# Kernel optimization log

Measured on AMD Instinct MI355X. Metric: run time of the kernel, lower is better.

Reference implementation:

```python
import jax, jax.numpy as jnp
import numpy as np

N_NODES = 100000
N_EDGES = 1600000
DIMS = [64, 64, 64, 32]  # [n_feat] + hid


def setup_inputs() -> dict:
    key = jax.random.key(0)
    ks = jax.random.split(key, 2 + 2 * (len(DIMS) - 1))
    x = jax.random.normal(ks[0], (N_NODES, DIMS[0]), dtype=jnp.float32)
    edge_index = jax.random.randint(ks[1], (2, N_EDGES), 0, N_NODES, dtype=jnp.int64)
    inp = {"x": x, "edge_index": edge_index}
    for i in range(len(DIMS) - 1):
        fan_in, fan_out = DIMS[i], DIMS[i + 1]
        scale = 1.0 / np.sqrt(fan_in)
        inp[f"W{i+1}"] = jax.random.normal(ks[2 + 2 * i], (fan_in, fan_out), dtype=jnp.float32) * scale
        inp[f"b{i+1}"] = jax.random.normal(ks[3 + 2 * i], (fan_out,), dtype=jnp.float32) * scale
    return inp


def _gcn_conv(x, W, b, src, dst, dis):
    # h = X W ; out[i] = sum_{j->i} norm_ij * h[j] + dis[i]^2 * h[i] + b
    h = x @ W
    norm = dis[src] * dis[dst]                      # [E]
    agg = jax.ops.segment_sum(h[src] * norm[:, None], dst, num_segments=x.shape[0])
    agg = agg + h * (dis * dis)[:, None]            # self-loop contribution
    return agg + b


def reference(x, edge_index, W1, b1, W2, b2, W3, b3):
    src, dst = edge_index[0], edge_index[1]
    n = x.shape[0]
    # degree with self-loops (edge weight 1), symmetric normalization
    deg = jax.ops.segment_sum(jnp.ones(src.shape[0], x.dtype), dst, num_segments=n) + 1.0
    dis = jax.lax.rsqrt(deg)
    h = jax.nn.relu(_gcn_conv(x, W1, b1, src, dst, dis))   # dropout is identity in eval
    h = jax.nn.relu(_gcn_conv(h, W2, b2, src, dst, dis))
    return _gcn_conv(h, W3, b3, src, dst, dis)
```

## Files before the change

### kernel.cpp

```cpp
#include <hip/hip_runtime.h>


typedef __attribute__((ext_vector_type(8))) _Float16 half8;
typedef __attribute__((ext_vector_type(4))) _Float16 half4;

static inline int cdiv(int a, int b) { return (a + b - 1) / b; }

#define ACHUNK 8192
#define MAXNBK 512

__global__ void k_bucket_hist(const int* __restrict__ dst, int* __restrict__ counts_t,
                              int NBK, int NBA, int E) {
    __shared__ int cnt[MAXNBK];
    int t = threadIdx.x, b = blockIdx.x;
    for (int i = t; i < NBK; i += 256) cnt[i] = 0;
    __syncthreads();
    int e0 = b * ACHUNK;
#pragma unroll 8
    for (int j = 0; j < ACHUNK / 256; ++j) {
        int e = e0 + j * 256 + t;
        if (e < E) atomicAdd(&cnt[dst[e] >> 8], 1);
    }
    __syncthreads();
    for (int i = t; i < NBK; i += 256) counts_t[i * NBA + b] = cnt[i];
}

#define SCAN_T 256
#define SCAN_V 4
#define SCAN_CHUNK 1024

__global__ void k_scan_partial(const int* __restrict__ a, int* __restrict__ bsum, int n) {
    __shared__ int red[SCAN_T];
    int t = threadIdx.x, b = blockIdx.x;
    int base = b * SCAN_CHUNK + t * SCAN_V;
    int s = 0;
#pragma unroll
    for (int j = 0; j < SCAN_V; ++j) { int i = base + j; if (i < n) s += a[i]; }
    red[t] = s;
    __syncthreads();
    for (int off = SCAN_T / 2; off > 0; off >>= 1) {
        if (t < off) red[t] += red[t + off];
        __syncthreads();
    }
    if (t == 0) bsum[b] = red[0];
}

__global__ void k_scan_final(const int* __restrict__ a, const int* __restrict__ bsum,
                             int* __restrict__ out, int nb, int n) {
    __shared__ int sb[256];
    __shared__ int sh[SCAN_T];
    int t = threadIdx.x, bk = blockIdx.x;
    sb[t] = (t < nb) ? bsum[t] : 0;
    __syncthreads();
    for (int off = 1; off < 256; off <<= 1) {
        int u = (t >= off) ? sb[t - off] : 0;
        __syncthreads();
        sb[t] += u;
        __syncthreads();
    }
    int bbase = (bk == 0) ? 0 : sb[bk - 1];
    int base = bk * SCAN_CHUNK + t * SCAN_V;
    int v[SCAN_V];
    int s = 0;
#pragma unroll
    for (int j = 0; j < SCAN_V; ++j) {
        int i = base + j;
        v[j] = (i < n) ? a[i] : 0;
        s += v[j];
    }
    sh[t] = s;
    __syncthreads();
    for (int off = 1; off < SCAN_T; off <<= 1) {
        int u = (t >= off) ? sh[t - off] : 0;
        __syncthreads();
        sh[t] += u;
        __syncthreads();
    }
    int run = sh[t] - s + bbase;
#pragma unroll
    for (int j = 0; j < SCAN_V; ++j) {
        int i = base + j;
        if (i < n) { out[i] = run; run += v[j]; }
    }
}

__global__ void k_bucket_scatter(const int* __restrict__ src, const int* __restrict__ dst,
                                 const int* __restrict__ offsets, unsigned* __restrict__ bucketed,
                                 int NBK, int NBA, int E) {
    __shared__ int curs[MAXNBK];
    int t = threadIdx.x, b = blockIdx.x;
    for (int i = t; i < NBK; i += 256) curs[i] = offsets[i * NBA + b];
    __syncthreads();
    int e0 = b * ACHUNK;
#pragma unroll 8
    for (int j = 0; j < ACHUNK / 256; ++j) {
        int e = e0 + j * 256 + t;
        if (e < E) {
            int d = dst[e];
            int pos = atomicAdd(&curs[d >> 8], 1);
            bucketed[pos] = (unsigned)src[e] | ((unsigned)(d & 255) << 24);
        }
    }
}

__global__ void k_bucket_build(const unsigned* __restrict__ bucketed,
                               const int* __restrict__ offsets,
                               int* __restrict__ csr_src, int* __restrict__ row_start,
                               float* __restrict__ dis, int NBK, int NBA, int N, int E) {
    __shared__ int cnt[256];
    __shared__ int sc[256];
    int t = threadIdx.x, k = blockIdx.x;
    int base = offsets[k * NBA];
    int end = (k + 1 < NBK) ? offsets[(k + 1) * NBA] : E;
    cnt[t] = 0;
    __syncthreads();
    for (int i = base + t; i < end; i += 256)
        atomicAdd(&cnt[bucketed[i] >> 24], 1);
    __syncthreads();
    int c = cnt[t];
    sc[t] = c;
    __syncthreads();
    for (int off = 1; off < 256; off <<= 1) {
        int u = (t >= off) ? sc[t - off] : 0;
        __syncthreads();
        sc[t] += u;
        __syncthreads();
    }
    int excl = sc[t] - c;
    int node = k * 256 + t;
    if (node < N) {
        row_start[node] = base + excl;
        dis[node] = rsqrtf(1.0f + (float)c);
    }
    if (k == 0 && t == 0) row_start[N] = E;
    cnt[t] = base + excl;
    __syncthreads();
    for (int i = base + t; i < end; i += 256) {
        unsigned w = bucketed[i];
        int pos = atomicAdd(&cnt[w >> 24], 1);
        csr_src[pos] = (int)(w & 0xFFFFFFu);
    }
}

template <int K, int M>
__global__ void k_gemm_f(const float* __restrict__ X, const float* __restrict__ W,
                         const float* __restrict__ dis, _Float16* __restrict__ H, int n) {
    constexpr int TPR = M / 8;
    constexpr int ROWS = 256 / TPR;
    constexpr int KP = K + 1;
    __shared__ float Ws[K * M];
    __shared__ float Xs[ROWS * KP];
    int tid = threadIdx.x;
    for (int idx = tid; idx < K * M / 4; idx += 256)
        ((float4*)Ws)[idx] = ((const float4*)W)[idx];
    int row0 = blockIdx.x * ROWS;
    for (int idx = tid; idx < ROWS * (K / 4); idx += 256) {
        int r = idx / (K / 4), kq = idx % (K / 4);
        int row = row0 + r;
        float4 vv = (row < n) ? ((const float4*)X)[(size_t)row * (K / 4) + kq]
                              : make_float4(0.f, 0.f, 0.f, 0.f);
        Xs[r * KP + kq * 4 + 0] = vv.x;
        Xs[r * KP + kq * 4 + 1] = vv.y;
        Xs[r * KP + kq * 4 + 2] = vv.z;
        Xs[r * KP + kq * 4 + 3] = vv.w;
    }
    __syncthreads();
    int r = tid / TPR, c0 = (tid % TPR) * 8;
    int row = row0 + r;
    if (row >= n) return;
    float4 a0 = make_float4(0.f, 0.f, 0.f, 0.f);
    float4 a1 = make_float4(0.f, 0.f, 0.f, 0.f);
#pragma unroll
    for (int k = 0; k < K; ++k) {
        float xv = Xs[r * KP + k];
        float4 w0 = ((const float4*)Ws)[(k * M + c0) / 4];
        float4 w1 = ((const float4*)Ws)[(k * M + c0) / 4 + 1];
        a0.x = fmaf(xv, w0.x, a0.x);
        a0.y = fmaf(xv, w0.y, a0.y);
        a0.z = fmaf(xv, w0.z, a0.z);
        a0.w = fmaf(xv, w0.w, a0.w);
        a1.x = fmaf(xv, w1.x, a1.x);
        a1.y = fmaf(xv, w1.y, a1.y);
        a1.z = fmaf(xv, w1.z, a1.z);
        a1.w = fmaf(xv, w1.w, a1.w);
    }
    float dn = dis[row];
    half8 hv;
    hv[0] = (_Float16)(a0.x * dn);
    hv[1] = (_Float16)(a0.y * dn);
    hv[2] = (_Float16)(a0.z * dn);
    hv[3] = (_Float16)(a0.w * dn);
    hv[4] = (_Float16)(a1.x * dn);
    hv[5] = (_Float16)(a1.y * dn);
    hv[6] = (_Float16)(a1.z * dn);
    hv[7] = (_Float16)(a1.w * dn);
    ((half8*)H)[(size_t)row * (M / 8) + c0 / 8] = hv;
}

template <int MOUT>
__global__ __launch_bounds__(256, 8)
void k_fused_agg_gemm(const _Float16* __restrict__ h, const float* __restrict__ dis,
                      const int* __restrict__ row_start, const int* __restrict__ csr_src,
                      const float* __restrict__ bagg, const float* __restrict__ W,
                      _Float16* __restrict__ H, int n) {
    constexpr int K = 64, KP = K + 1;
    __shared__ __align__(16) _Float16 Ws[K * MOUT];
    __shared__ float Xs[32 * KP];
    int tid = threadIdx.x;
    for (int idx = tid; idx < K * MOUT / 4; idx += 256) {
        float4 wv = ((const float4*)W)[idx];
        half4 h4;
        h4[0] = (_Float16)wv.x;
        h4[1] = (_Float16)wv.y;
        h4[2] = (_Float16)wv.z;
        h4[3] = (_Float16)wv.w;
        ((half4*)Ws)[idx] = h4;
    }

    int wave = tid >> 6, lane = tid & 63;
    int sub = lane >> 3, fl = lane & 7;
    int node0 = blockIdx.x * 32;
    int node = node0 + wave * 8 + sub;
    if (node < n) {
        const half8* h8 = (const half8*)h;
        float acc[8];
#pragma unroll
        for (int j = 0; j < 8; ++j) acc[j] = 0.f;
        int e = row_start[node], e1 = row_start[node + 1];
        for (; e + 7 < e1; e += 8) {
            int s0 = csr_src[e], s1 = csr_src[e + 1];
            int s2 = csr_src[e + 2], s3 = csr_src[e + 3];
// ... 16 lines not shown
            int s0 = csr_src[e], s1 = csr_src[e + 1];
            int s2 = csr_src[e + 2], s3 = csr_src[e + 3];
            half8 v0 = h8[(size_t)s0 * 8 + fl];
            half8 v1 = h8[(size_t)s1 * 8 + fl];
            half8 v2 = h8[(size_t)s2 * 8 + fl];
            half8 v3 = h8[(size_t)s3 * 8 + fl];
#pragma unroll
            for (int j = 0; j < 8; ++j)
                acc[j] += ((float)v0[j] + (float)v1[j]) + ((float)v2[j] + (float)v3[j]);
        }
        for (; e < e1; ++e) {
            int s0 = csr_src[e];
            half8 v0 = h8[(size_t)s0 * 8 + fl];
#pragma unroll
            for (int j = 0; j < 8; ++j) acc[j] += (float)v0[j];
        }
        float dn = dis[node];
        half8 hv = h8[(size_t)node * 8 + fl];
        float4 b0 = ((const float4*)bagg)[fl * 2];
        float4 b1 = ((const float4*)bagg)[fl * 2 + 1];
        int rrow = wave * 8 + sub;
        float* xp = &Xs[rrow * KP + fl * 8];
        xp[0] = fmaxf((acc[0] + (float)hv[0]) * dn + b0.x, 0.f);
        xp[1] = fmaxf((acc[1] + (float)hv[1]) * dn + b0.y, 0.f);
        xp[2] = fmaxf((acc[2] + (float)hv[2]) * dn + b0.z, 0.f);
        xp[3] = fmaxf((acc[3] + (float)hv[3]) * dn + b0.w, 0.f);
        xp[4] = fmaxf((acc[4] + (float)hv[4]) * dn + b1.x, 0.f);
        xp[5] = fmaxf((acc[5] + (float)hv[5]) * dn + b1.y, 0.f);
        xp[6] = fmaxf((acc[6] + (float)hv[6]) * dn + b1.z, 0.f);
        xp[7] = fmaxf((acc[7] + (float)hv[7]) * dn + b1.w, 0.f);
    }
    __syncthreads();

    constexpr int TPR = MOUT / 8;
    int r = tid / TPR, c0 = (tid % TPR) * 8;
    int row = node0 + r;
    if (r >= 32 || row >= n) return;
    float4 a0 = make_float4(0.f, 0.f, 0.f, 0.f);
    float4 a1 = make_float4(0.f, 0.f, 0.f, 0.f);
#pragma unroll
    for (int k = 0; k < K; ++k) {
        float xv = Xs[r * KP + k];
        half8 w = ((const half8*)Ws)[(k * MOUT + c0) / 8];
        a0.x = fmaf(xv, (float)w[0], a0.x);
        a0.y = fmaf(xv, (float)w[1], a0.y);
        a0.z = fmaf(xv, (float)w[2], a0.z);
        a0.w = fmaf(xv, (float)w[3], a0.w);
        a1.x = fmaf(xv, (float)w[4], a1.x);
        a1.y = fmaf(xv, (float)w[5], a1.y);
        a1.z = fmaf(xv, (float)w[6], a1.z);
        a1.w = fmaf(xv, (float)w[7], a1.w);
    }
    float dn = dis[row];
    half8 hv;
    hv[0] = (_Float16)(a0.x * dn);
    hv[1] = (_Float16)(a0.y * dn);
    hv[2] = (_Float16)(a0.z * dn);
    hv[3] = (_Float16)(a0.w * dn);
    hv[4] = (_Float16)(a1.x * dn);
    hv[5] = (_Float16)(a1.y * dn);
    hv[6] = (_Float16)(a1.z * dn);
    hv[7] = (_Float16)(a1.w * dn);
    ((half8*)H)[(size_t)row * (MOUT / 8) + c0 / 8] = hv;
}

__global__ __launch_bounds__(256, 8)
void k_aggregate32(const _Float16* __restrict__ h, const float* __restrict__ dis,
                   const int* __restrict__ row_start, const int* __restrict__ csr_src,
                   const float* __restrict__ b, float* __restrict__ out, int n) {
    constexpr int LPN = 4, NPW = 16;
    int gtid = blockIdx.x * blockDim.x + threadIdx.x;
    int wave = gtid >> 6;
    int lane = threadIdx.x & 63;
    int sub = lane / LPN, fl = lane % LPN;
    int node = wave * NPW + sub;
    if (node >= n) return;
    const half8* h8 = (const half8*)h;
    float acc[8];
#pragma unroll
    for (int j = 0; j < 8; ++j) acc[j] = 0.f;
    int e = row_start[node], e1 = row_start[node + 1];
    for (; e + 7 < e1; e += 8) {
        int s0 = csr_src[e], s1 = csr_src[e + 1];
        int s2 = csr_src[e + 2], s3 = csr_src[e + 3];
        int s4 = csr_src[e + 4], s5 = csr_src[e + 5];
        int s6 = csr_src[e + 6], s7 = csr_src[e + 7];
        half8 v0 = h8[(size_t)s0 * LPN + fl];
        half8 v1 = h8[(size_t)s1 * LPN + fl];
        half8 v2 = h8[(size_t)s2 * LPN + fl];
        half8 v3 = h8[(size_t)s3 * LPN + fl];
        half8 v4 = h8[(size_t)s4 * LPN + fl];
        half8 v5 = h8[(size_t)s5 * LPN + fl];
        half8 v6 = h8[(size_t)s6 * LPN + fl];
        half8 v7 = h8[(size_t)s7 * LPN + fl];
#pragma unroll
        for (int j = 0; j < 8; ++j)
// ... 20 lines not shown
    float dn = dis[node];
    half8 hv = h8[(size_t)node * LPN + fl];
    float4 b0 = ((const float4*)b)[fl * 2];
    float4 b1 = ((const float4*)b)[fl * 2 + 1];
    float4* op = (float4*)(out + ((size_t)node * LPN + fl) * 8);
    op[0] = make_float4((acc[0] + (float)hv[0]) * dn + b0.x,
                        (acc[1] + (float)hv[1]) * dn + b0.y,
                        (acc[2] + (float)hv[2]) * dn + b0.z,
                        (acc[3] + (float)hv[3]) * dn + b0.w);
    op[1] = make_float4((acc[4] + (float)hv[4]) * dn + b1.x,
                        (acc[5] + (float)hv[5]) * dn + b1.y,
                        (acc[6] + (float)hv[6]) * dn + b1.z,
                        (acc[7] + (float)hv[7]) * dn + b1.w);
}

extern "C" void kernel_launch(void* const* d_in, const int* in_sizes, int n_in,
                              void* d_out, int out_size, void* d_ws, size_t ws_size,
                              hipStream_t stream) {
    const float* x   = (const float*)d_in[0];
    const int*   ei  = (const int*)d_in[1];
    const float* W1  = (const float*)d_in[2];
    const float* b1  = (const float*)d_in[3];
    const float* W2  = (const float*)d_in[4];
    const float* b2  = (const float*)d_in[5];
    const float* W3  = (const float*)d_in[6];
    const float* b3  = (const float*)d_in[7];
    float* out = (float*)d_out;

    const int N = in_sizes[0] / 64;
    const int E = in_sizes[1] / 2;
    const int* src = ei;
    const int* dst = ei + E;

    const int NBK = cdiv(N, 256);
    const int NBA = cdiv(E, ACHUNK);
    const int nmat = NBK * NBA;

    const size_t Np = (size_t)((N + 63) / 64) * 64;
    char* p = (char*)d_ws;
    int*      counts_t = (int*)p;      p += (size_t)nmat * sizeof(int);
    int*      offsets  = (int*)p;      p += (size_t)nmat * sizeof(int);
    int*      bsum     = (int*)p;      p += 1024 * sizeof(int);
    int*      row_start= (int*)p;      p += (Np + 64) * sizeof(int);
    float*    dis      = (float*)p;    p += Np * sizeof(float);
    unsigned* bucketed = (unsigned*)p; p += (size_t)E * sizeof(unsigned);
    int*      csr_src  = (int*)p;      p += (size_t)E * sizeof(int);
    _Float16* bufA     = (_Float16*)p; p += Np * 64 * sizeof(_Float16);
    _Float16* bufB     = (_Float16*)p; p += Np * 64 * sizeof(_Float16);
    (void)ws_size;

    const int B = 256;
    const int nb = cdiv(nmat, SCAN_CHUNK);

    k_bucket_hist<<<NBA, B, 0, stream>>>(dst, counts_t, NBK, NBA, E);
    k_scan_partial<<<nb, B, 0, stream>>>(counts_t, bsum, nmat);
    k_scan_final<<<nb, B, 0, stream>>>(counts_t, bsum, offsets, nb, nmat);
    k_bucket_scatter<<<NBA, B, 0, stream>>>(src, dst, offsets, bucketed, NBK, NBA, E);
    k_bucket_build<<<NBK, B, 0, stream>>>(bucketed, offsets, csr_src, row_start, dis,
                                          NBK, NBA, N, E);

    k_gemm_f<64, 64><<<cdiv(N, 32), B, 0, stream>>>(x, W1, dis, bufA, N);
    k_fused_agg_gemm<64><<<cdiv(N, 32), B, 0, stream>>>(
        bufA, dis, row_start, csr_src, b1, W2, bufB, N);
    k_fused_agg_gemm<32><<<cdiv(N, 32), B, 0, stream>>>(
        bufB, dis, row_start, csr_src, b2, W3, bufA, N);
    k_aggregate32<<<cdiv(cdiv(N, 16) * 64, B), B, 0, stream>>>(
        bufA, dis, row_start, csr_src, b3, out, N);
}
```

Measured before the change: 302.2 us.

## Fuse CSR construction and first GEMM into one cooperative persistent kernel

Replaces the six separate kernels (histogram, two scan passes, bucket scatter, bucket build, first-layer GEMM) with one cooperative kernel that uses grid.sync between phases, aiming to cut launch and inter-kernel drain overhead. The bucket build now sorts each bucket in shared memory and writes csr_src coalesced, falling back to direct scatter for buckets too large to fit. The 32-output fused agg-gemm now uses all 256 threads with 4 columns each instead of leaving half the threads idle. Risks: the persistent grid may reduce parallelism in some phases, and each grid-wide barrier has its own cost.

```diff
diff --git a/kernel.cpp b/kernel.cpp
--- a/kernel.cpp
+++ b/kernel.cpp
@@ -1,5 +1,8 @@
 #include <hip/hip_runtime.h>
-
+#include <hip/hip_cooperative_groups.h>
+
+
+namespace cg = cooperative_groups;
 
 typedef __attribute__((ext_vector_type(8))) _Float16 half8;
 typedef __attribute__((ext_vector_type(4))) _Float16 half4;
@@ -8,6 +11,229 @@
 
 #define ACHUNK 8192
 #define MAXNBK 512
+#define SCAN_CHUNK 1024
+#define BCAP 6144
+#define SMEM_BYTES 26624
+
+__global__ __launch_bounds__(256)
+void k_csr_gemm(const int* __restrict__ src, const int* __restrict__ dst,
+                int* __restrict__ counts_t, int* __restrict__ offsets,
+                int* __restrict__ bsum, unsigned* __restrict__ bucketed,
+                int* __restrict__ csr_src, int* __restrict__ row_start,
+                float* __restrict__ dis, const float* __restrict__ X,
+                const float* __restrict__ W1, _Float16* __restrict__ H,
+                int NBK, int NBA, int nmat, int nb, int N, int E) {
+    cg::grid_group grid = cg::this_grid();
+    __shared__ __align__(16) char smem[SMEM_BYTES];
+    const int t = threadIdx.x;
+    const int nbl = gridDim.x;
+
+    {
+        int* cnt = (int*)smem;
+        for (int c = blockIdx.x; c < NBA; c += nbl) {
+            for (int i = t; i < NBK; i += 256) cnt[i] = 0;
+            __syncthreads();
+            int e0 = c * ACHUNK;
+#pragma unroll 8
+            for (int j = 0; j < ACHUNK / 256; ++j) {
+                int e = e0 + j * 256 + t;
+                if (e < E) atomicAdd(&cnt[dst[e] >> 8], 1);
+            }
+            __syncthreads();
+            for (int i = t; i < NBK; i += 256) counts_t[i * NBA + c] = cnt[i];
+            __syncthreads();
+        }
+    }
+    grid.sync();
+
+    {
+        int* red = (int*)smem;
+        for (int b = blockIdx.x; b < nb; b += nbl) {
+            int base = b * SCAN_CHUNK + t * 4;
+            int s = 0;
+#pragma unroll
+            for (int j = 0; j < 4; ++j) { int i = base + j; if (i < nmat) s += counts_t[i]; }
+            red[t] = s;
+            __syncthreads();
+            for (int off = 128; off > 0; off >>= 1) {
+                if (t < off) red[t] += red[t + off];
+                __syncthreads();
+            }
+            if (t == 0) bsum[b] = red[0];
+            __syncthreads();
+        }
+    }
+    grid.sync();
+
+    {
+        int* sb = (int*)smem;
+        int* sh = sb + 256;
+        for (int bk = blockIdx.x; bk < nb; bk += nbl) {
+            sb[t] = (t < nb) ? bsum[t] : 0;
+            __syncthreads();
+            for (int off = 1; off < 256; off <<= 1) {
+                int u = (t >= off) ? sb[t - off] : 0;
+                __syncthreads();
+                sb[t] += u;
+                __syncthreads();
+            }
+            int bbase = (bk == 0) ? 0 : sb[bk - 1];
+            int base = bk * SCAN_CHUNK + t * 4;
+            int v[4];
+            int s = 0;
+#pragma unroll
+            for (int j = 0; j < 4; ++j) {
+                int i = base + j;
+                v[j] = (i < nmat) ? counts_t[i] : 0;
+                s += v[j];
+            }
+            sh[t] = s;
+            __syncthreads();
+            for (int off = 1; off < 256; off <<= 1) {
+                int u = (t >= off) ? sh[t - off] : 0;
+                __syncthreads();
+                sh[t] += u;
+                __syncthreads();
+            }
+            int run = sh[t] - s + bbase;
+#pragma unroll
+            for (int j = 0; j < 4; ++j) {
+                int i = base + j;
+                if (i < nmat) { offsets[i] = run; run += v[j]; }
+            }
+            __syncthreads();
+        }
+    }
+    grid.sync();
+
+    {
+        int* curs = (int*)smem;
+        for (int c = blockIdx.x; c < NBA; c += nbl) {
+            for (int i = t; i < NBK; i += 256) curs[i] = offsets[i * NBA + c];
+            __syncthreads();
+            int e0 = c * ACHUNK;
+#pragma unroll 8
+            for (int j = 0; j < ACHUNK / 256; ++j) {
+                int e = e0 + j * 256 + t;
+                if (e < E) {
+                    int d = dst[e];
+                    int pos = atomicAdd(&curs[d >> 8], 1);
+                    bucketed[pos] = (unsigned)src[e] | ((unsigned)(d & 255) << 24);
+                }
+            }
+            __syncthreads();
+        }
+    }
+    grid.sync();
+
+    {
+        int* cnt = (int*)smem;
+        int* sc  = cnt + 256;
+        int* srt = sc + 256;
+        for (int k = blockIdx.x; k < NBK; k += nbl) {
+            int base = offsets[k * NBA];
+            int end = (k + 1 < NBK) ? offsets[(k + 1) * NBA] : E;
+            cnt[t] = 0;
+            __syncthreads();
+            for (int i = base + t; i < end; i += 256)
+                atomicAdd(&cnt[bucketed[i] >> 24], 1);
+            __syncthreads();
+            int c = cnt[t];
+            sc[t] = c;
+            __syncthreads();
+            for (int off = 1; off < 256; off <<= 1) {
+                int u = (t >= off) ? sc[t - off] : 0;
+                __syncthreads();
+                sc[t] += u;
+                __syncthreads();
+            }
+            int excl = sc[t] - c;
+            int node = k * 256 + t;
+            if (node < N) {
+                row_start[node] = base + excl;
+                dis[node] = rsqrtf(1.0f + (float)c);
+            }
+            if (k == 0 && t == 0) row_start[N] = E;
+            cnt[t] = excl;
+            __syncthreads();
+            int m = end - base;
+            if (m <= BCAP) {
+                for (int i = base + t; i < end; i += 256) {
+                    unsigned w = bucketed[i];
+                    int r = atomicAdd(&cnt[w >> 24], 1);
+                    srt[r] = (int)(w & 0xFFFFFFu);
+                }
+                __syncthreads();
+                for (int idx = t; idx < m; idx += 256)
+                    csr_src[base + idx] = srt[idx];
+            } else {
+                for (int i = base + t; i < end; i += 256) {
+                    unsigned w = bucketed[i];
+                    int pos = base + atomicAdd(&cnt[w >> 24], 1);
+                    csr_src[pos] = (int)(w & 0xFFFFFFu);
+                }
+            }
+            __syncthreads();
+        }
+    }
+    grid.sync();
+
+    {
+        float* Ws = (float*)smem;
+        float* Xs = Ws + 64 * 64;
+        constexpr int K = 64, KP = 65;
+        for (int idx = t; idx < K * 64 / 4; idx += 256)
+            ((float4*)Ws)[idx] = ((const float4*)W1)[idx];
+        int ntile = (N + 31) / 32;
+        int r = t / 8, c0 = (t % 8) * 8;
+        for (int tile = blockIdx.x; tile < ntile; tile += nbl) {
+            int row0 = tile * 32;
+            for (int idx = t; idx < 32 * (K / 4); idx += 256) {
+                int rr = idx / (K / 4), kq = idx % (K / 4);
+                int row = row0 + rr;
+                float4 vv = (row < N) ? ((const float4*)X)[(size_t)row * (K / 4) + kq]
+                                      : make_float4(0.f, 0.f, 0.f, 0.f);
+                Xs[rr * KP + kq * 4 + 0] = vv.x;
+                Xs[rr * KP + kq * 4 + 1] = vv.y;
+                Xs[rr * KP + kq * 4 + 2] = vv.z;
+                Xs[rr * KP + kq * 4 + 3] = vv.w;
+            }
+            __syncthreads();
+            int row = row0 + r;
+            if (row < N) {
+                float4 a0 = make_float4(0.f, 0.f, 0.f, 0.f);
+                float4 a1 = make_float4(0.f, 0.f, 0.f, 0.f);
+#pragma unroll
+                for (int k = 0; k < K; ++k) {
+                    float xv = Xs[r * KP + k];
+                    float4 w0 = ((const float4*)Ws)[(k * 64 + c0) / 4];
+                    float4 w1 = ((const float4*)Ws)[(k * 64 + c0) / 4 + 1];
+                    a0.x = fmaf(xv, w0.x, a0.x);
+                    a0.y = fmaf(xv, w0.y, a0.y);
+                    a0.z = fmaf(xv, w0.z, a0.z);
+                    a0.w = fmaf(xv, w0.w, a0.w);
+                    a1.x = fmaf(xv, w1.x, a1.x);
+                    a1.y = fmaf(xv, w1.y, a1.y);
+                    a1.z = fmaf(xv, w1.z, a1.z);
+                    a1.w = fmaf(xv, w1.w, a1.w);
+                }
+                float dn = dis[row];
+                half8 hv;
+                hv[0] = (_Float16)(a0.x * dn);
+                hv[1] = (_Float16)(a0.y * dn);
+                hv[2] = (_Float16)(a0.z * dn);
+                hv[3] = (_Float16)(a0.w * dn);
+                hv[4] = (_Float16)(a1.x * dn);
+                hv[5] = (_Float16)(a1.y * dn);
+                hv[6] = (_Float16)(a1.z * dn);
+                hv[7] = (_Float16)(a1.w * dn);
+                ((half8*)H)[(size_t)row * 8 + c0 / 8] = hv;
+            }
+            __syncthreads();
+        }
+    }
+}
+
 
 __global__ void k_bucket_hist(const int* __restrict__ dst, int* __restrict__ counts_t,
                               int NBK, int NBA, int E) {
@@ -25,20 +251,16 @@
     for (int i = t; i < NBK; i += 256) counts_t[i * NBA + b] = cnt[i];
 }
 
-#define SCAN_T 256
-#define SCAN_V 4
-#define SCAN_CHUNK 1024
-
 __global__ void k_scan_partial(const int* __restrict__ a, int* __restrict__ bsum, int n) {
-    __shared__ int red[SCAN_T];
+    __shared__ int red[256];
     int t = threadIdx.x, b = blockIdx.x;
-    int base = b * SCAN_CHUNK + t * SCAN_V;
+    int base = b * SCAN_CHUNK + t * 4;
     int s = 0;
 #pragma unroll
-    for (int j = 0; j < SCAN_V; ++j) { int i = base + j; if (i < n) s += a[i]; }
+    for (int j = 0; j < 4; ++j) { int i = base + j; if (i < n) s += a[i]; }
     red[t] = s;
     __syncthreads();
-    for (int off = SCAN_T / 2; off > 0; off >>= 1) {
+    for (int off = 128; off > 0; off >>= 1) {
         if (t < off) red[t] += red[t + off];
         __syncthreads();
     }
@@ -48,7 +270,7 @@
 __global__ void k_scan_final(const int* __restrict__ a, const int* __restrict__ bsum,
                              int* __restrict__ out, int nb, int n) {
     __shared__ int sb[256];
-    __shared__ int sh[SCAN_T];
+    __shared__ int sh[256];
     int t = threadIdx.x, bk = blockIdx.x;
     sb[t] = (t < nb) ? bsum[t] : 0;
     __syncthreads();
@@ -59,18 +281,18 @@
         __syncthreads();
     }
     int bbase = (bk == 0) ? 0 : sb[bk - 1];
-    int base = bk * SCAN_CHUNK + t * SCAN_V;
-    int v[SCAN_V];
+    int base = bk * SCAN_CHUNK + t * 4;
+    int v[4];
     int s = 0;
 #pragma unroll
-    for (int j = 0; j < SCAN_V; ++j) {
+    for (int j = 0; j < 4; ++j) {
         int i = base + j;
         v[j] = (i < n) ? a[i] : 0;
         s += v[j];
     }
     sh[t] = s;
     __syncthreads();
-    for (int off = 1; off < SCAN_T; off <<= 1) {
+    for (int off = 1; off < 256; off <<= 1) {
         int u = (t >= off) ? sh[t - off] : 0;
         __syncthreads();
         sh[t] += u;
@@ -78,7 +300,7 @@
     }
     int run = sh[t] - s + bbase;
 #pragma unroll
-    for (int j = 0; j < SCAN_V; ++j) {
+    for (int j = 0; j < 4; ++j) {
         int i = base + j;
         if (i < n) { out[i] = run; run += v[j]; }
     }
@@ -109,6 +331,7 @@
                                float* __restrict__ dis, int NBK, int NBA, int N, int E) {
     __shared__ int cnt[256];
     __shared__ int sc[256];
+    __shared__ int srt[BCAP];
     int t = threadIdx.x, k = blockIdx.x;
     int base = offsets[k * NBA];
     int end = (k + 1 < NBK) ? offsets[(k + 1) * NBA] : E;
@@ -133,12 +356,24 @@
         dis[node] = rsqrtf(1.0f + (float)c);
     }
     if (k == 0 && t == 0) row_start[N] = E;
-    cnt[t] = base + excl;
-    __syncthreads();
-    for (int i = base + t; i < end; i += 256) {
-        unsigned w = bucketed[i];
-        int pos = atomicAdd(&cnt[w >> 24], 1);
-        csr_src[pos] = (int)(w & 0xFFFFFFu);
+    cnt[t] = excl;
+    __syncthreads();
+    int m = end - base;
+    if (m <= BCAP) {
+        for (int i = base + t; i < end; i += 256) {
+            unsigned w = bucketed[i];
+            int r = atomicAdd(&cnt[w >> 24], 1);
+            srt[r] = (int)(w & 0xFFFFFFu);
+        }
+        __syncthreads();
+        for (int idx = t; idx < m; idx += 256)
+            csr_src[base + idx] = srt[idx];
+    } else {
+        for (int i = base + t; i < end; i += 256) {
+            unsigned w = bucketed[i];
+            int pos = base + atomicAdd(&cnt[w >> 24], 1);
+            csr_src[pos] = (int)(w & 0xFFFFFFu);
+        }
     }
 }
 
@@ -197,6 +432,7 @@
     ((half8*)H)[(size_t)row * (M / 8) + c0 / 8] = hv;
 }
 
+
 template <int MOUT>
 __global__ __launch_bounds__(256, 8)
 void k_fused_agg_gemm(const _Float16* __restrict__ h, const float* __restrict__ dis,
@@ -279,36 +515,54 @@
     }
     __syncthreads();
 
-    constexpr int TPR = MOUT / 8;
-    int r = tid / TPR, c0 = (tid % TPR) * 8;
+    constexpr int TPR = 8;
+    constexpr int CPT = MOUT / TPR;
+    int r = tid / TPR, c0 = (tid % TPR) * CPT;
     int row = node0 + r;
-    if (r >= 32 || row >= n) return;
+    if (row >= n) return;
     float4 a0 = make_float4(0.f, 0.f, 0.f, 0.f);
     float4 a1 = make_float4(0.f, 0.f, 0.f, 0.f);
 #pragma unroll
     for (int k = 0; k < K; ++k) {
         float xv = Xs[r * KP + k];
-        half8 w = ((const half8*)Ws)[(k * MOUT + c0) / 8];
-        a0.x = fmaf(xv, (float)w[0], a0.x);
-        a0.y = fmaf(xv, (float)w[1], a0.y);
-        a0.z = fmaf(xv, (float)w[2], a0.z);
-        a0.w = fmaf(xv, (float)w[3], a0.w);
-        a1.x = fmaf(xv, (float)w[4], a1.x);
-        a1.y = fmaf(xv, (float)w[5], a1.y);
-        a1.z = fmaf(xv, (float)w[6], a1.z);
-        a1.w = fmaf(xv, (float)w[7], a1.w);
+        if constexpr (CPT == 8) {
+            half8 w = ((const half8*)Ws)[(k * MOUT + c0) / 8];
+            a0.x = fmaf(xv, (float)w[0], a0.x);
+            a0.y = fmaf(xv, (float)w[1], a0.y);
+            a0.z = fmaf(xv, (float)w[2], a0.z);
+            a0.w = fmaf(xv, (float)w[3], a0.w);
+            a1.x = fmaf(xv, (float)w[4], a1.x);
+            a1.y = fmaf(xv, (float)w[5], a1.y);
+            a1.z = fmaf(xv, (float)w[6], a1.z);
+            a1.w = fmaf(xv, (float)w[7], a1.w);
+        } else {
+            half4 w = ((const half4*)Ws)[(k * MOUT + c0) / 4];
+            a0.x = fmaf(xv, (float)w[0], a0.x);
+            a0.y = fmaf(xv, (float)w[1], a0.y);
+            a0.z = fmaf(xv, (float)w[2], a0.z);
+            a0.w = fmaf(xv, (float)w[3], a0.w);
+        }
     }
     float dn = dis[row];
-    half8 hv;
-    hv[0] = (_Float16)(a0.x * dn);
-    hv[1] = (_Float16)(a0.y * dn);
-    hv[2] = (_Float16)(a0.z * dn);
-    hv[3] = (_Float16)(a0.w * dn);
-    hv[4] = (_Float16)(a1.x * dn);
-    hv[5] = (_Float16)(a1.y * dn);
-    hv[6] = (_Float16)(a1.z * dn);
-    hv[7] = (_Float16)(a1.w * dn);
-    ((half8*)H)[(size_t)row * (MOUT / 8) + c0 / 8] = hv;
+    if constexpr (CPT == 8) {
+        half8 hv;
+        hv[0] = (_Float16)(a0.x * dn);
+        hv[1] = (_Float16)(a0.y * dn);
+        hv[2] = (_Float16)(a0.z * dn);
+        hv[3] = (_Float16)(a0.w * dn);
+        hv[4] = (_Float16)(a1.x * dn);
+        hv[5] = (_Float16)(a1.y * dn);
+        hv[6] = (_Float16)(a1.z * dn);
+        hv[7] = (_Float16)(a1.w * dn);
+        ((half8*)H)[(size_t)row * (MOUT / 8) + c0 / 8] = hv;
+    } else {
+        half4 hv;
+        hv[0] = (_Float16)(a0.x * dn);
+        hv[1] = (_Float16)(a0.y * dn);
+        hv[2] = (_Float16)(a0.z * dn);
+        hv[3] = (_Float16)(a0.w * dn);
+        ((half4*)H)[(size_t)row * (MOUT / 4) + c0 / 4] = hv;
+    }
 }
 
 __global__ __launch_bounds__(256, 8)
@@ -398,6 +652,7 @@
     const int NBK = cdiv(N, 256);
     const int NBA = cdiv(E, ACHUNK);
     const int nmat = NBK * NBA;
+    const int nb = cdiv(nmat, SCAN_CHUNK);
 
     const size_t Np = (size_t)((N + 63) / 64) * 64;
     char* p = (char*)d_ws;
@@ -413,16 +668,50 @@
     (void)ws_size;
 
     const int B = 256;
-    const int nb = cdiv(nmat, SCAN_CHUNK);
-
-    k_bucket_hist<<<NBA, B, 0, stream>>>(dst, counts_t, NBK, NBA, E);
-    k_scan_partial<<<nb, B, 0, stream>>>(counts_t, bsum, nmat);
-    k_scan_final<<<nb, B, 0, stream>>>(counts_t, bsum, offsets, nb, nmat);
-    k_bucket_scatter<<<NBA, B, 0, stream>>>(src, dst, offsets, bucketed, NBK, NBA, E);
-    k_bucket_build<<<NBK, B, 0, stream>>>(bucketed, offsets, csr_src, row_start, dis,
-                                          NBK, NBA, N, E);
-
-    k_gemm_f<64, 64><<<cdiv(N, 32), B, 0, stream>>>(x, W1, dis, bufA, N);
+
+    static int coop_grid = -1;
+    if (coop_grid < 0) {
+        int dev = 0;
+        (void)hipGetDevice(&dev);
+        int ncu = 0;
+        (void)hipDeviceGetAttribute(&ncu, hipDeviceAttributeMultiprocessorCount, dev);
+        int maxb = 0;
+        (void)hipOccupancyMaxActiveBlocksPerMultiprocessor(
+            &maxb, (const void*)k_csr_gemm, B, 0);
+        long g = (long)maxb * (long)ncu;
+        if (g > 1024) g = 1024;
+        coop_grid = (int)g;
+    }
+
+    if (coop_grid >= 64) {
+        const int* src_a = src;
+        const int* dst_a = dst;
+        int* counts_a = counts_t;
+        int* offsets_a = offsets;
+        int* bsum_a = bsum;
+        unsigned* bucketed_a = bucketed;
+        int* csr_a = csr_src;
+        int* rs_a = row_start;
+        float* dis_a = dis;
+        const float* x_a = x;
+        const float* w1_a = W1;
+        _Float16* h_a = bufA;
+        int nbk_a = NBK, nba_a = NBA, nmat_a = nmat, nb_a = nb, n_a = N, e_a = E;
+        void* args[] = {&src_a, &dst_a, &counts_a, &offsets_a, &bsum_a,
+                        &bucketed_a, &csr_a, &rs_a, &dis_a, &x_a, &w1_a, &h_a,
+                        &nbk_a, &nba_a, &nmat_a, &nb_a, &n_a, &e_a};
+        hipLaunchCooperativeKernel((void*)k_csr_gemm, dim3(coop_grid), dim3(B),
+                                   args, 0, stream);
+    } else {
+        k_bucket_hist<<<NBA, B, 0, stream>>>(dst, counts_t, NBK, NBA, E);
+        k_scan_partial<<<nb, B, 0, stream>>>(counts_t, bsum, nmat);
+        k_scan_final<<<nb, B, 0, stream>>>(counts_t, bsum, offsets, nb, nmat);
+        k_bucket_scatter<<<NBA, B, 0, stream>>>(src, dst, offsets, bucketed, NBK, NBA, E);
+        k_bucket_build<<<NBK, B, 0, stream>>>(bucketed, offsets, csr_src, row_start, dis,
+                                              NBK, NBA, N, E);
+        k_gemm_f<64, 64><<<cdiv(N, 32), B, 0, stream>>>(x, W1, dis, bufA, N);
+    }
+
     k_fused_agg_gemm<64><<<cdiv(N, 32), B, 0, stream>>>(
         bufA, dis, row_start, csr_src, b1, W2, bufB, N);
     k_fused_agg_gemm<32><<<cdiv(N, 32), B, 0, stream>>>(
```

After: 706.7 us. 134% more time.

## Replace two-level bucketed CSR build with direct global-atomic degree count and scatter

Applied to the files above, without the earlier changes.

Replaces the bucket histogram/scatter/build pipeline with a per-node degree count using global atomics, a scan over nodes that also writes row_start, cursor and dis, and a direct scatter of src into CSR via atomic cursors. This drops the intermediate bucketed array and one pass over the edges. In exchange it relies on many scattered global atomics, and the order of neighbours within each row is no longer deterministic. It also changes the output-GEMM thread mapping in the fused aggregate kernel to 8 threads per row, so the MOUT=32 case uses all 256 threads with 4 columns each instead of leaving half idle.

```diff
diff --git a/kernel.cpp b/kernel.cpp
--- a/kernel.cpp
+++ b/kernel.cpp
@@ -6,49 +6,42 @@
 
 static inline int cdiv(int a, int b) { return (a + b - 1) / b; }
 
-#define ACHUNK 8192
-#define MAXNBK 512
-
-__global__ void k_bucket_hist(const int* __restrict__ dst, int* __restrict__ counts_t,
-                              int NBK, int NBA, int E) {
-    __shared__ int cnt[MAXNBK];
+#define SCAN_CHUNK 1024
+
+__global__ __launch_bounds__(256)
+void k_deg(const int* __restrict__ dst, int* __restrict__ deg, int E) {
+    int t = threadIdx.x;
+    int base = blockIdx.x * 1024;
+#pragma unroll
+    for (int j = 0; j < 4; ++j) {
+        int e = base + j * 256 + t;
+        if (e < E) atomicAdd(&deg[dst[e]], 1);
+    }
+}
+
+__global__ __launch_bounds__(256)
+void k_scan_partial(const int* __restrict__ a, int* __restrict__ bsum, int n) {
+    __shared__ int red[256];
     int t = threadIdx.x, b = blockIdx.x;
-    for (int i = t; i < NBK; i += 256) cnt[i] = 0;
-    __syncthreads();
-    int e0 = b * ACHUNK;
-#pragma unroll 8
-    for (int j = 0; j < ACHUNK / 256; ++j) {
-        int e = e0 + j * 256 + t;
-        if (e < E) atomicAdd(&cnt[dst[e] >> 8], 1);
-    }
-    __syncthreads();
-    for (int i = t; i < NBK; i += 256) counts_t[i * NBA + b] = cnt[i];
-}
-
-#define SCAN_T 256
-#define SCAN_V 4
-#define SCAN_CHUNK 1024
-
-__global__ void k_scan_partial(const int* __restrict__ a, int* __restrict__ bsum, int n) {
-    __shared__ int red[SCAN_T];
-    int t = threadIdx.x, b = blockIdx.x;
-    int base = b * SCAN_CHUNK + t * SCAN_V;
+    int base = b * SCAN_CHUNK + t * 4;
     int s = 0;
 #pragma unroll
-    for (int j = 0; j < SCAN_V; ++j) { int i = base + j; if (i < n) s += a[i]; }
+    for (int j = 0; j < 4; ++j) { int i = base + j; if (i < n) s += a[i]; }
     red[t] = s;
     __syncthreads();
-    for (int off = SCAN_T / 2; off > 0; off >>= 1) {
+    for (int off = 128; off > 0; off >>= 1) {
         if (t < off) red[t] += red[t + off];
         __syncthreads();
     }
     if (t == 0) bsum[b] = red[0];
 }
 
-__global__ void k_scan_final(const int* __restrict__ a, const int* __restrict__ bsum,
-                             int* __restrict__ out, int nb, int n) {
+__global__ __launch_bounds__(256)
+void k_scan_final(const int* __restrict__ deg, const int* __restrict__ bsum,
+                  int* __restrict__ row_start, int* __restrict__ cursor,
+                  float* __restrict__ dis, int nb, int n, int E) {
     __shared__ int sb[256];
-    __shared__ int sh[SCAN_T];
+    __shared__ int sh[256];
     int t = threadIdx.x, bk = blockIdx.x;
     sb[t] = (t < nb) ? bsum[t] : 0;
     __syncthreads();
@@ -59,18 +52,18 @@
         __syncthreads();
     }
     int bbase = (bk == 0) ? 0 : sb[bk - 1];
-    int base = bk * SCAN_CHUNK + t * SCAN_V;
-    int v[SCAN_V];
+    int base = bk * SCAN_CHUNK + t * 4;
+    int v[4];
     int s = 0;
 #pragma unroll
-    for (int j = 0; j < SCAN_V; ++j) {
+    for (int j = 0; j < 4; ++j) {
         int i = base + j;
-        v[j] = (i < n) ? a[i] : 0;
+        v[j] = (i < n) ? deg[i] : 0;
         s += v[j];
     }
     sh[t] = s;
     __syncthreads();
-    for (int off = 1; off < SCAN_T; off <<= 1) {
+    for (int off = 1; off < 256; off <<= 1) {
         int u = (t >= off) ? sh[t - off] : 0;
         __syncthreads();
         sh[t] += u;
@@ -78,67 +71,32 @@
     }
     int run = sh[t] - s + bbase;
 #pragma unroll
-    for (int j = 0; j < SCAN_V; ++j) {
+    for (int j = 0; j < 4; ++j) {
         int i = base + j;
-        if (i < n) { out[i] = run; run += v[j]; }
-    }
-}
-
-__global__ void k_bucket_scatter(const int* __restrict__ src, const int* __restrict__ dst,
-                                 const int* __restrict__ offsets, unsigned* __restrict__ bucketed,
-                                 int NBK, int NBA, int E) {
-    __shared__ int curs[MAXNBK];
-    int t = threadIdx.x, b = blockIdx.x;
-    for (int i = t; i < NBK; i += 256) curs[i] = offsets[i * NBA + b];
-    __syncthreads();
-    int e0 = b * ACHUNK;
-#pragma unroll 8
-    for (int j = 0; j < ACHUNK / 256; ++j) {
-        int e = e0 + j * 256 + t;
+        if (i < n) {
+            row_start[i] = run;
+            cursor[i] = run;
+            dis[i] = rsqrtf(1.0f + (float)v[j]);
+            if (i == n - 1) row_start[n] = run + v[j];
+            run += v[j];
+        }
+    }
+}
+
+__global__ __launch_bounds__(256)
+void k_scatter_direct(const int* __restrict__ src, const int* __restrict__ dst,
+                      int* __restrict__ cursor, int* __restrict__ csr_src, int E) {
+    int t = threadIdx.x;
+    int base = blockIdx.x * 1024;
+#pragma unroll
+    for (int j = 0; j < 4; ++j) {
+        int e = base + j * 256 + t;
         if (e < E) {
             int d = dst[e];
-            int pos = atomicAdd(&curs[d >> 8], 1);
-            bucketed[pos] = (unsigned)src[e] | ((unsigned)(d & 255) << 24);
-        }
-    }
-}
-
-__global__ void k_bucket_build(const unsigned* __restrict__ bucketed,
-                               const int* __restrict__ offsets,
-                               int* __restrict__ csr_src, int* __restrict__ row_start,
-                               float* __restrict__ dis, int NBK, int NBA, int N, int E) {
-    __shared__ int cnt[256];
-    __shared__ int sc[256];
-    int t = threadIdx.x, k = blockIdx.x;
-    int base = offsets[k * NBA];
-    int end = (k + 1 < NBK) ? offsets[(k + 1) * NBA] : E;
-    cnt[t] = 0;
-    __syncthreads();
-    for (int i = base + t; i < end; i += 256)
-        atomicAdd(&cnt[bucketed[i] >> 24], 1);
-    __syncthreads();
-    int c = cnt[t];
-    sc[t] = c;
-    __syncthreads();
-    for (int off = 1; off < 256; off <<= 1) {
-        int u = (t >= off) ? sc[t - off] : 0;
-        __syncthreads();
-        sc[t] += u;
-        __syncthreads();
-    }
-    int excl = sc[t] - c;
-    int node = k * 256 + t;
-    if (node < N) {
-        row_start[node] = base + excl;
-        dis[node] = rsqrtf(1.0f + (float)c);
-    }
-    if (k == 0 && t == 0) row_start[N] = E;
-    cnt[t] = base + excl;
-    __syncthreads();
-    for (int i = base + t; i < end; i += 256) {
-        unsigned w = bucketed[i];
-        int pos = atomicAdd(&cnt[w >> 24], 1);
-        csr_src[pos] = (int)(w & 0xFFFFFFu);
+            int s = src[e];
+            int pos = atomicAdd(&cursor[d], 1);
+            csr_src[pos] = s;
+        }
     }
 }
 
@@ -279,36 +237,54 @@
     }
     __syncthreads();
 
-    constexpr int TPR = MOUT / 8;
-    int r = tid / TPR, c0 = (tid % TPR) * 8;
+    constexpr int TPR = 8;
+    constexpr int CPT = MOUT / TPR;
+    int r = tid / TPR, c0 = (tid % TPR) * CPT;
     int row = node0 + r;
-    if (r >= 32 || row >= n) return;
+    if (row >= n) return;
     float4 a0 = make_float4(0.f, 0.f, 0.f, 0.f);
     float4 a1 = make_float4(0.f, 0.f, 0.f, 0.f);
 #pragma unroll
     for (int k = 0; k < K; ++k) {
         float xv = Xs[r * KP + k];
-        half8 w = ((const half8*)Ws)[(k * MOUT + c0) / 8];
-        a0.x = fmaf(xv, (float)w[0], a0.x);
-        a0.y = fmaf(xv, (float)w[1], a0.y);
-        a0.z = fmaf(xv, (float)w[2], a0.z);
-        a0.w = fmaf(xv, (float)w[3], a0.w);
-        a1.x = fmaf(xv, (float)w[4], a1.x);
-        a1.y = fmaf(xv, (float)w[5], a1.y);
-        a1.z = fmaf(xv, (float)w[6], a1.z);
-        a1.w = fmaf(xv, (float)w[7], a1.w);
+        if constexpr (CPT == 8) {
+            half8 w = ((const half8*)Ws)[(k * MOUT + c0) / 8];
+            a0.x = fmaf(xv, (float)w[0], a0.x);
+            a0.y = fmaf(xv, (float)w[1], a0.y);
+            a0.z = fmaf(xv, (float)w[2], a0.z);
+            a0.w = fmaf(xv, (float)w[3], a0.w);
+            a1.x = fmaf(xv, (float)w[4], a1.x);
+            a1.y = fmaf(xv, (float)w[5], a1.y);
+            a1.z = fmaf(xv, (float)w[6], a1.z);
+            a1.w = fmaf(xv, (float)w[7], a1.w);
+        } else {
+            half4 w = ((const half4*)Ws)[(k * MOUT + c0) / 4];
+            a0.x = fmaf(xv, (float)w[0], a0.x);
+            a0.y = fmaf(xv, (float)w[1], a0.y);
+            a0.z = fmaf(xv, (float)w[2], a0.z);
+            a0.w = fmaf(xv, (float)w[3], a0.w);
+        }
     }
     float dn = dis[row];
-    half8 hv;
-    hv[0] = (_Float16)(a0.x * dn);
-    hv[1] = (_Float16)(a0.y * dn);
-    hv[2] = (_Float16)(a0.z * dn);
-    hv[3] = (_Float16)(a0.w * dn);
-    hv[4] = (_Float16)(a1.x * dn);
-    hv[5] = (_Float16)(a1.y * dn);
-    hv[6] = (_Float16)(a1.z * dn);
-    hv[7] = (_Float16)(a1.w * dn);
-    ((half8*)H)[(size_t)row * (MOUT / 8) + c0 / 8] = hv;
+    if constexpr (CPT == 8) {
+        half8 hv;
+        hv[0] = (_Float16)(a0.x * dn);
+        hv[1] = (_Float16)(a0.y * dn);
+        hv[2] = (_Float16)(a0.z * dn);
+        hv[3] = (_Float16)(a0.w * dn);
+        hv[4] = (_Float16)(a1.x * dn);
+        hv[5] = (_Float16)(a1.y * dn);
+        hv[6] = (_Float16)(a1.z * dn);
+        hv[7] = (_Float16)(a1.w * dn);
+        ((half8*)H)[(size_t)row * (MOUT / 8) + c0 / 8] = hv;
+    } else {
+        half4 hv;
+        hv[0] = (_Float16)(a0.x * dn);
+        hv[1] = (_Float16)(a0.y * dn);
+        hv[2] = (_Float16)(a0.z * dn);
+        hv[3] = (_Float16)(a0.w * dn);
+        ((half4*)H)[(size_t)row * (MOUT / 4) + c0 / 4] = hv;
+    }
 }
 
 __global__ __launch_bounds__(256, 8)
@@ -395,34 +371,28 @@
     const int* src = ei;
     const int* dst = ei + E;
 
-    const int NBK = cdiv(N, 256);
-    const int NBA = cdiv(E, ACHUNK);
-    const int nmat = NBK * NBA;
-
     const size_t Np = (size_t)((N + 63) / 64) * 64;
     char* p = (char*)d_ws;
-    int*      counts_t = (int*)p;      p += (size_t)nmat * sizeof(int);
-    int*      offsets  = (int*)p;      p += (size_t)nmat * sizeof(int);
+    int*      deg      = (int*)p;      p += Np * sizeof(int);
+    int*      row_start= (int*)p;      p += (Np + 64) * sizeof(int);
+    int*      cursor   = (int*)p;      p += Np * sizeof(int);
+    float*    dis      = (float*)p;    p += Np * sizeof(float);
     int*      bsum     = (int*)p;      p += 1024 * sizeof(int);
-    int*      row_start= (int*)p;      p += (Np + 64) * sizeof(int);
-    float*    dis      = (float*)p;    p += Np * sizeof(float);
-    unsigned* bucketed = (unsigned*)p; p += (size_t)E * sizeof(unsigned);
     int*      csr_src  = (int*)p;      p += (size_t)E * sizeof(int);
     _Float16* bufA     = (_Float16*)p; p += Np * 64 * sizeof(_Float16);
     _Float16* bufB     = (_Float16*)p; p += Np * 64 * sizeof(_Float16);
     (void)ws_size;
 
     const int B = 256;
-    const int nb = cdiv(nmat, SCAN_CHUNK);
-
-    k_bucket_hist<<<NBA, B, 0, stream>>>(dst, counts_t, NBK, NBA, E);
-    k_scan_partial<<<nb, B, 0, stream>>>(counts_t, bsum, nmat);
-    k_scan_final<<<nb, B, 0, stream>>>(counts_t, bsum, offsets, nb, nmat);
-    k_bucket_scatter<<<NBA, B, 0, stream>>>(src, dst, offsets, bucketed, NBK, NBA, E);
-    k_bucket_build<<<NBK, B, 0, stream>>>(bucketed, offsets, csr_src, row_start, dis,
-                                          NBK, NBA, N, E);
-
+    const int nb2 = cdiv(N, SCAN_CHUNK);
+
+    hipMemsetAsync(deg, 0, (size_t)N * sizeof(int), stream);
+    k_deg<<<cdiv(E, 1024), B, 0, stream>>>(dst, deg, E);
+    k_scan_partial<<<nb2, B, 0, stream>>>(deg, bsum, N);
+    k_scan_final<<<nb2, B, 0, stream>>>(deg, bsum, row_start, cursor, dis, nb2, N, E);
     k_gemm_f<64, 64><<<cdiv(N, 32), B, 0, stream>>>(x, W1, dis, bufA, N);
+    k_scatter_direct<<<cdiv(E, 1024), B, 0, stream>>>(src, dst, cursor, csr_src, E);
+
     k_fused_agg_gemm<64><<<cdiv(N, 32), B, 0, stream>>>(
         bufA, dis, row_start, csr_src, b1, W2, bufB, N);
     k_fused_agg_gemm<32><<<cdiv(N, 32), B, 0, stream>>>(
```

Measured after the change: 417.9 us. +38.3%, slower.

## Shrink dst buckets, sort within LDS, and retile fused GEMM output threads

Applied to the files above, without the earlier changes.

Dst buckets shrink from 256 to 128 nodes, and edge chunks shrink from 8192 to 2048 edges, giving more parallel blocks. The scan now handles up to 1024 block sums so the larger count matrix still fits. k_bucket_build first sorts each bucket's sources into a shared-memory buffer and then writes csr_src with coalesced stores, keeping a global-scatter fallback for buckets larger than the buffer. The fused agg+GEMM output stage now uses 8 threads per row, so the MOUT=32 variant keeps all 256 threads busy with half4 outputs instead of leaving half the block idle. The costs are a much larger count matrix to scan and extra shared memory in the build kernel.

```diff
diff --git a/kernel.cpp b/kernel.cpp
--- a/kernel.cpp
+++ b/kernel.cpp
@@ -6,11 +6,16 @@
 
 static inline int cdiv(int a, int b) { return (a + b - 1) / b; }
 
-#define ACHUNK 8192
-#define MAXNBK 512
-
-__global__ void k_bucket_hist(const int* __restrict__ dst, int* __restrict__ counts_t,
-                              int NBK, int NBA, int E) {
+#define ACHUNK 2048
+#define BSHIFT 7
+#define BMASK 127
+#define MAXNBK 1024
+#define SCAN_CHUNK 1024
+#define BCAP 4096
+
+__global__ __launch_bounds__(256)
+void k_bucket_hist(const int* __restrict__ dst, int* __restrict__ counts_t,
+                   int NBK, int NBA, int E) {
     __shared__ int cnt[MAXNBK];
     int t = threadIdx.x, b = blockIdx.x;
     for (int i = t; i < NBK; i += 256) cnt[i] = 0;
@@ -19,58 +24,79 @@
 #pragma unroll 8
     for (int j = 0; j < ACHUNK / 256; ++j) {
         int e = e0 + j * 256 + t;
-        if (e < E) atomicAdd(&cnt[dst[e] >> 8], 1);
+        if (e < E) atomicAdd(&cnt[dst[e] >> BSHIFT], 1);
     }
     __syncthreads();
     for (int i = t; i < NBK; i += 256) counts_t[i * NBA + b] = cnt[i];
 }
 
-#define SCAN_T 256
-#define SCAN_V 4
-#define SCAN_CHUNK 1024
-
-__global__ void k_scan_partial(const int* __restrict__ a, int* __restrict__ bsum, int n) {
-    __shared__ int red[SCAN_T];
+__global__ __launch_bounds__(256)
+void k_scan_partial(const int* __restrict__ a, int* __restrict__ bsum, int n) {
+    __shared__ int red[256];
     int t = threadIdx.x, b = blockIdx.x;
-    int base = b * SCAN_CHUNK + t * SCAN_V;
+    int base = b * SCAN_CHUNK + t * 4;
     int s = 0;
 #pragma unroll
-    for (int j = 0; j < SCAN_V; ++j) { int i = base + j; if (i < n) s += a[i]; }
+    for (int j = 0; j < 4; ++j) { int i = base + j; if (i < n) s += a[i]; }
     red[t] = s;
     __syncthreads();
-    for (int off = SCAN_T / 2; off > 0; off >>= 1) {
+    for (int off = 128; off > 0; off >>= 1) {
         if (t < off) red[t] += red[t + off];
         __syncthreads();
     }
     if (t == 0) bsum[b] = red[0];
 }
 
-__global__ void k_scan_final(const int* __restrict__ a, const int* __restrict__ bsum,
-                             int* __restrict__ out, int nb, int n) {
-    __shared__ int sb[256];
-    __shared__ int sh[SCAN_T];
+__global__ __launch_bounds__(256)
+void k_scan_final(const int* __restrict__ a, const int* __restrict__ bsum,
+                  int* __restrict__ out, int nb, int n) {
+    __shared__ int sh[256];
+    __shared__ int bb;
     int t = threadIdx.x, bk = blockIdx.x;
-    sb[t] = (t < nb) ? bsum[t] : 0;
+    int bv[4];
+    int bt = 0;
+#pragma unroll
+    for (int j = 0; j < 4; ++j) {
+        int i = 4 * t + j;
+        bv[j] = (i < nb) ? bsum[i] : 0;
+        bt += bv[j];
+    }
+    sh[t] = bt;
     __syncthreads();
     for (int off = 1; off < 256; off <<= 1) {
-        int u = (t >= off) ? sb[t - off] : 0;
-        __syncthreads();
-        sb[t] += u;
-        __syncthreads();
-    }
-    int bbase = (bk == 0) ? 0 : sb[bk - 1];
-    int base = bk * SCAN_CHUNK + t * SCAN_V;
-    int v[SCAN_V];
+        int u = (t >= off) ? sh[t - off] : 0;
+        __syncthreads();
+        sh[t] += u;
+        __syncthreads();
+    }
+    int bexcl = sh[t] - bt;
+    if (bk == 0) {
+        if (t == 0) bb = 0;
+    } else {
+        int q = bk - 1;
+        if (t == (q >> 2)) {
+            int s = bexcl;
+#pragma unroll
+            for (int j = 0; j < 4; ++j)
+                if (j <= (q & 3)) s += bv[j];
+            bb = s;
+        }
+    }
+    __syncthreads();
+    int bbase = bb;
+    __syncthreads();
+    int base = bk * SCAN_CHUNK + t * 4;
+    int v[4];
     int s = 0;
 #pragma unroll
-    for (int j = 0; j < SCAN_V; ++j) {
+    for (int j = 0; j < 4; ++j) {
         int i = base + j;
         v[j] = (i < n) ? a[i] : 0;
         s += v[j];
     }
     sh[t] = s;
     __syncthreads();
-    for (int off = 1; off < SCAN_T; off <<= 1) {
+    for (int off = 1; off < 256; off <<= 1) {
         int u = (t >= off) ? sh[t - off] : 0;
         __syncthreads();
         sh[t] += u;
@@ -78,15 +104,16 @@
     }
     int run = sh[t] - s + bbase;
 #pragma unroll
-    for (int j = 0; j < SCAN_V; ++j) {
+    for (int j = 0; j < 4; ++j) {
         int i = base + j;
         if (i < n) { out[i] = run; run += v[j]; }
     }
 }
 
-__global__ void k_bucket_scatter(const int* __restrict__ src, const int* __restrict__ dst,
-                                 const int* __restrict__ offsets, unsigned* __restrict__ bucketed,
-                                 int NBK, int NBA, int E) {
+__global__ __launch_bounds__(256)
+void k_bucket_scatter(const int* __restrict__ src, const int* __restrict__ dst,
+                      const int* __restrict__ offsets, unsigned* __restrict__ bucketed,
+                      int NBK, int NBA, int E) {
     __shared__ int curs[MAXNBK];
     int t = threadIdx.x, b = blockIdx.x;
     for (int i = t; i < NBK; i += 256) curs[i] = offsets[i * NBA + b];
@@ -97,48 +124,64 @@
         int e = e0 + j * 256 + t;
         if (e < E) {
             int d = dst[e];
-            int pos = atomicAdd(&curs[d >> 8], 1);
-            bucketed[pos] = (unsigned)src[e] | ((unsigned)(d & 255) << 24);
-        }
-    }
-}
-
-__global__ void k_bucket_build(const unsigned* __restrict__ bucketed,
-                               const int* __restrict__ offsets,
-                               int* __restrict__ csr_src, int* __restrict__ row_start,
-                               float* __restrict__ dis, int NBK, int NBA, int N, int E) {
-    __shared__ int cnt[256];
-    __shared__ int sc[256];
+            int pos = atomicAdd(&curs[d >> BSHIFT], 1);
+            bucketed[pos] = (unsigned)src[e] | ((unsigned)(d & BMASK) << 24);
+        }
+    }
+}
+
+__global__ __launch_bounds__(256)
+void k_bucket_build(const unsigned* __restrict__ bucketed,
+                    const int* __restrict__ offsets,
+                    int* __restrict__ csr_src, int* __restrict__ row_start,
+                    float* __restrict__ dis, int NBK, int NBA, int N, int E) {
+    __shared__ int cnt[128];
+    __shared__ int sc[128];
+    __shared__ int srt[BCAP];
     int t = threadIdx.x, k = blockIdx.x;
     int base = offsets[k * NBA];
     int end = (k + 1 < NBK) ? offsets[(k + 1) * NBA] : E;
-    cnt[t] = 0;
+    if (t < 128) cnt[t] = 0;
     __syncthreads();
     for (int i = base + t; i < end; i += 256)
         atomicAdd(&cnt[bucketed[i] >> 24], 1);
     __syncthreads();
-    int c = cnt[t];
-    sc[t] = c;
-    __syncthreads();
-    for (int off = 1; off < 256; off <<= 1) {
-        int u = (t >= off) ? sc[t - off] : 0;
-        __syncthreads();
-        sc[t] += u;
-        __syncthreads();
-    }
-    int excl = sc[t] - c;
-    int node = k * 256 + t;
-    if (node < N) {
-        row_start[node] = base + excl;
-        dis[node] = rsqrtf(1.0f + (float)c);
+    int c = 0;
+    if (t < 128) { c = cnt[t]; sc[t] = c; }
+    __syncthreads();
+    for (int off = 1; off < 128; off <<= 1) {
+        int u = (t >= off && t < 128) ? sc[t - off] : 0;
+        __syncthreads();
+        if (t < 128) sc[t] += u;
+        __syncthreads();
+    }
+    if (t < 128) {
+        int excl = sc[t] - c;
+        int node = (k << BSHIFT) + t;
+        if (node < N) {
+            row_start[node] = base + excl;
+            dis[node] = rsqrtf(1.0f + (float)c);
+        }
+        cnt[t] = excl;
     }
     if (k == 0 && t == 0) row_start[N] = E;
-    cnt[t] = base + excl;
-    __syncthreads();
-    for (int i = base + t; i < end; i += 256) {
-        unsigned w = bucketed[i];
-        int pos = atomicAdd(&cnt[w >> 24], 1);
-        csr_src[pos] = (int)(w & 0xFFFFFFu);
+    __syncthreads();
+    int m = end - base;
+    if (m <= BCAP) {
+        for (int i = base + t; i < end; i += 256) {
+            unsigned w = bucketed[i];
+            int r = atomicAdd(&cnt[w >> 24], 1);
+            srt[r] = (int)(w & 0xFFFFFFu);
+        }
+        __syncthreads();
+        for (int idx = t; idx < m; idx += 256)
+            csr_src[base + idx] = srt[idx];
+    } else {
+        for (int i = base + t; i < end; i += 256) {
+            unsigned w = bucketed[i];
+            int pos = base + atomicAdd(&cnt[w >> 24], 1);
+            csr_src[pos] = (int)(w & 0xFFFFFFu);
+        }
     }
 }
 
@@ -279,36 +322,54 @@
     }
     __syncthreads();
 
-    constexpr int TPR = MOUT / 8;
-    int r = tid / TPR, c0 = (tid % TPR) * 8;
+    constexpr int TPR = 8;
+    constexpr int CPT = MOUT / TPR;
+    int r = tid / TPR, c0 = (tid % TPR) * CPT;
     int row = node0 + r;
-    if (r >= 32 || row >= n) return;
+    if (row >= n) return;
     float4 a0 = make_float4(0.f, 0.f, 0.f, 0.f);
     float4 a1 = make_float4(0.f, 0.f, 0.f, 0.f);
 #pragma unroll
     for (int k = 0; k < K; ++k) {
         float xv = Xs[r * KP + k];
-        half8 w = ((const half8*)Ws)[(k * MOUT + c0) / 8];
-        a0.x = fmaf(xv, (float)w[0], a0.x);
-        a0.y = fmaf(xv, (float)w[1], a0.y);
-        a0.z = fmaf(xv, (float)w[2], a0.z);
-        a0.w = fmaf(xv, (float)w[3], a0.w);
-        a1.x = fmaf(xv, (float)w[4], a1.x);
-        a1.y = fmaf(xv, (float)w[5], a1.y);
-        a1.z = fmaf(xv, (float)w[6], a1.z);
-        a1.w = fmaf(xv, (float)w[7], a1.w);
+        if constexpr (CPT == 8) {
+            half8 w = ((const half8*)Ws)[(k * MOUT + c0) / 8];
+            a0.x = fmaf(xv, (float)w[0], a0.x);
+            a0.y = fmaf(xv, (float)w[1], a0.y);
+            a0.z = fmaf(xv, (float)w[2], a0.z);
+            a0.w = fmaf(xv, (float)w[3], a0.w);
+            a1.x = fmaf(xv, (float)w[4], a1.x);
+            a1.y = fmaf(xv, (float)w[5], a1.y);
+            a1.z = fmaf(xv, (float)w[6], a1.z);
+            a1.w = fmaf(xv, (float)w[7], a1.w);
+        } else {
+            half4 w = ((const half4*)Ws)[(k * MOUT + c0) / 4];
+            a0.x = fmaf(xv, (float)w[0], a0.x);
+            a0.y = fmaf(xv, (float)w[1], a0.y);
+            a0.z = fmaf(xv, (float)w[2], a0.z);
+            a0.w = fmaf(xv, (float)w[3], a0.w);
+        }
     }
     float dn = dis[row];
-    half8 hv;
-    hv[0] = (_Float16)(a0.x * dn);
-    hv[1] = (_Float16)(a0.y * dn);
-    hv[2] = (_Float16)(a0.z * dn);
-    hv[3] = (_Float16)(a0.w * dn);
-    hv[4] = (_Float16)(a1.x * dn);
-    hv[5] = (_Float16)(a1.y * dn);
-    hv[6] = (_Float16)(a1.z * dn);
-    hv[7] = (_Float16)(a1.w * dn);
-    ((half8*)H)[(size_t)row * (MOUT / 8) + c0 / 8] = hv;
+    if constexpr (CPT == 8) {
+        half8 hv;
+        hv[0] = (_Float16)(a0.x * dn);
+        hv[1] = (_Float16)(a0.y * dn);
+        hv[2] = (_Float16)(a0.z * dn);
+        hv[3] = (_Float16)(a0.w * dn);
+        hv[4] = (_Float16)(a1.x * dn);
+        hv[5] = (_Float16)(a1.y * dn);
+        hv[6] = (_Float16)(a1.z * dn);
+        hv[7] = (_Float16)(a1.w * dn);
+        ((half8*)H)[(size_t)row * (MOUT / 8) + c0 / 8] = hv;
+    } else {
+        half4 hv;
+        hv[0] = (_Float16)(a0.x * dn);
+        hv[1] = (_Float16)(a0.y * dn);
+        hv[2] = (_Float16)(a0.z * dn);
+        hv[3] = (_Float16)(a0.w * dn);
+        ((half4*)H)[(size_t)row * (MOUT / 4) + c0 / 4] = hv;
+    }
 }
 
 __global__ __launch_bounds__(256, 8)
@@ -395,9 +456,10 @@
     const int* src = ei;
     const int* dst = ei + E;
 
-    const int NBK = cdiv(N, 256);
+    const int NBK = cdiv(N, 128);
     const int NBA = cdiv(E, ACHUNK);
     const int nmat = NBK * NBA;
+    const int nb = cdiv(nmat, SCAN_CHUNK);
 
     const size_t Np = (size_t)((N + 63) / 64) * 64;
     char* p = (char*)d_ws;
@@ -413,7 +475,6 @@
     (void)ws_size;
 
     const int B = 256;
-    const int nb = cdiv(nmat, SCAN_CHUNK);
 
     k_bucket_hist<<<NBA, B, 0, stream>>>(dst, counts_t, NBK, NBA, E);
     k_scan_partial<<<nb, B, 0, stream>>>(counts_t, bsum, nmat);
```

Result: no change. 296.7 us, median of 2 (-1.8%).
